# Optimization experiments

Hardware: AMD Instinct MI355X
Metric: run time of the kernel (lower is better)

## Reference

```python
import jax, jax.numpy as jnp
import numpy as np

TAU = 0.7
# Dellar moment flip under x<->y swap: (rho, jy, jx, Pyy, Pxy, Pxx, N, Jy, Jx)
FLIP = np.array([0, 2, 1, 5, 4, 3, 6, 8, 7])


def _dellar_matrices():
    # D2Q9 velocities in lettuce stencil order
    e = np.array([[0, 0], [1, 0], [0, 1], [-1, 0], [0, -1],
                  [1, 1], [-1, 1], [-1, -1], [1, -1]], dtype=np.float64)
    ex, ey = e[:, 0], e[:, 1]
    g = np.array([1, -2, -2, -2, -2, 4, 4, 4, 4], dtype=np.float64)  # Dellar ghost mode
    third = 1.0 / 3.0
    M = np.stack([
        np.ones(9),            # rho
        ex,                    # jx
        ey,                    # jy
        ex * ex - third,       # Pxx - cs^2 rho
        ex * ey,               # Pxy
        ey * ey - third,       # Pyy - cs^2 rho
        g,                     # N (ghost)
        g * ex,                # Jx (ghost)
        g * ey,                # Jy (ghost)
    ])
    return M, np.linalg.inv(M)


def _mlp(x, w1, b1, w2, b2):
    # x: (nx, ny, 9) -> (nx, ny, 1); Linear(9,24) + ReLU + Linear(24,1)
    h = jax.nn.relu(jnp.einsum('xyi,oi->xyo', x, w1) + b1)
    return jnp.einsum('xyo,po->xyp', h, w2) + b2


def setup_inputs() -> dict:
    key = jax.random.key(0)
    ks = jax.random.split(key, 9)
    nx = ny = 2048
    f = jax.random.uniform(ks[0], (9, nx, ny), dtype=jnp.float32)

    def lin_w(k, o, i):
        return jax.random.uniform(k, (o, i), dtype=jnp.float32,
                                  minval=-1.0, maxval=1.0) / np.sqrt(i)

    def lin_b(k, o, i):
        return jax.random.uniform(k, (o,), dtype=jnp.float32,
                                  minval=-1.0, maxval=1.0) / np.sqrt(i)

    M, Minv = _dellar_matrices()
    return {
        'f': f,
        'j_w1': lin_w(ks[1], 24, 9), 'j_b1': lin_b(ks[2], 24, 9),
        'j_w2': lin_w(ks[3], 1, 24), 'j_b2': lin_b(ks[4], 1, 24),
        'n_w1': lin_w(ks[5], 24, 9), 'n_b1': lin_b(ks[6], 24, 9),
        'n_w2': lin_w(ks[7], 1, 24), 'n_b2': lin_b(ks[8], 1, 24),
        'M': jnp.asarray(M, jnp.float32),
        'Minv': jnp.asarray(Minv, jnp.float32),
    }


def reference(f, j_w1, j_b1, j_w2, j_b2, n_w1, n_b1, n_w2, n_b2, M, Minv):
    # moment transform: m_i = M_ij f_j, shape (9, nx, ny)
    m = jnp.einsum('ij,jxy->ixy', M, f)
    mt = jnp.transpose(m, (1, 2, 0))        # (nx, ny, 9)
    mtf = mt[..., FLIP]                     # x<->y flipped moments

    gt_half = lambda a: 0.5 + jnp.exp(a)
    tau_jx = gt_half(_mlp(mt, j_w1, j_b1, j_w2, j_b2))[..., 0]
    tau_jy = gt_half(_mlp(mtf, j_w1, j_b1, j_w2, j_b2))[..., 0]
    tau_n = gt_half(_mlp(mt, n_w1, n_b1, n_w2, n_b2)
                    + _mlp(mtf, n_w1, n_b1, n_w2, n_b2))[..., 0]

    taus = jnp.full_like(m, TAU)
    taus = taus.at[6].set(tau_n).at[7].set(tau_jx).at[8].set(tau_jy)

    rho, jx, jy = m[0], m[1], m[2]
    zero = jnp.zeros_like(rho)
    meq = jnp.stack([rho, jx, jy,
                     jx * jx / rho, jx * jy / rho, jy * jy / rho,
                     zero, zero, zero])

    m_post = m - (m - meq) / taus
    return jnp.einsum('ij,jxy->ixy', Minv, m_post)
```

## Files before the change

### kernel.cpp

```cpp
#include <hip/hip_runtime.h>

typedef float f32x2 __attribute__((ext_vector_type(2)));

__device__ __forceinline__ f32x2 splat2(float s) { f32x2 v; v.x = s; v.y = s; return v; }
__device__ __forceinline__ f32x2 pfma(f32x2 a, f32x2 b, f32x2 c) { return __builtin_elementwise_fma(a, b, c); }
__device__ __forceinline__ f32x2 pfmas(float a, f32x2 b, f32x2 c) { return __builtin_elementwise_fma(splat2(a), b, c); }
__device__ __forceinline__ f32x2 prelu(f32x2 a) { return __builtin_elementwise_max(a, splat2(0.0f)); }

#define NP 2

__global__ __launch_bounds__(256) void mrt_kernel(
    const float* __restrict__ f,
    const float* __restrict__ j_w1, const float* __restrict__ j_b1,
    const float* __restrict__ j_w2, const float* __restrict__ j_b2,
    const float* __restrict__ n_w1, const float* __restrict__ n_b1,
    const float* __restrict__ n_w2, const float* __restrict__ n_b2,
    const float* __restrict__ Mg, const float* __restrict__ Minvg,
    float* __restrict__ out, int n2)
{
    __shared__ __align__(16) float sW[24][20];
    __shared__ float sW2[24][2];
    __shared__ float sMt[9][9];
    __shared__ float sMv[9][9];
    __shared__ float sb2[2];

    const int tid = threadIdx.x;

    if (tid < 48) {
        const int o = tid >> 1;
        const int which = tid & 1;
        const float* w1 = which ? n_w1 : j_w1;
        const float* b1 = which ? n_b1 : j_b1;
        float w[9];
        #pragma unroll
        for (int i = 0; i < 9; ++i) w[i] = w1[o * 9 + i];
        float* dst = &sW[o][which * 10];
        dst[0] = w[0]; dst[1] = w[4]; dst[2] = w[6];
        dst[3] = 0.5f * (w[1] + w[2]); dst[4] = 0.5f * (w[3] + w[5]); dst[5] = 0.5f * (w[7] + w[8]);
        dst[6] = 0.5f * (w[1] - w[2]); dst[7] = 0.5f * (w[3] - w[5]); dst[8] = 0.5f * (w[7] - w[8]);
        dst[9] = b1[o];
        if (which == 0) { sW2[o][0] = j_w2[o]; sW2[o][1] = n_w2[o]; }
    }
    for (int t = tid; t < 81; t += 256) {
        sMt[t % 9][t / 9] = Mg[t];
        sMv[t / 9][t % 9] = Minvg[t];
    }
    if (tid == 0) { sb2[0] = j_b2[0]; sb2[1] = n_b2[0]; }
    __syncthreads();

    const long base = ((long)blockIdx.x * blockDim.x + tid) * (2 * NP);
    if (base >= n2) return;

    f32x2 m[NP][9];
    #pragma unroll
    for (int p = 0; p < NP; ++p)
        #pragma unroll
        for (int r = 0; r < 9; ++r) m[p][r] = splat2(0.0f);

    #pragma unroll
    for (int i = 0; i < 9; ++i) {
        const float4 v = *reinterpret_cast<const float4*>(f + (size_t)i * n2 + base);
        f32x2 v0; v0.x = v.x; v0.y = v.y;
        f32x2 v1; v1.x = v.z; v1.y = v.w;
        #pragma unroll
        for (int r = 0; r < 9; ++r) {
            const float w = sMt[i][r];
            m[0][r] = pfmas(w, v0, m[0][r]);
            m[1][r] = pfmas(w, v1, m[1][r]);
        }
    }

    f32x2 tv[NP][9];
    #pragma unroll
    for (int p = 0; p < NP; ++p) {
        tv[p][0] = m[p][0]; tv[p][1] = m[p][4]; tv[p][2] = m[p][6];
        tv[p][3] = m[p][1] + m[p][2]; tv[p][4] = m[p][3] + m[p][5]; tv[p][5] = m[p][7] + m[p][8];
        tv[p][6] = m[p][1] - m[p][2]; tv[p][7] = m[p][3] - m[p][5]; tv[p][8] = m[p][7] - m[p][8];
    }

    f32x2 accj[NP], accjf[NP], accn[NP];
    #pragma unroll
    for (int p = 0; p < NP; ++p) { accj[p] = splat2(0.f); accjf[p] = splat2(0.f); accn[p] = splat2(0.f); }

    #pragma unroll 4
    for (int o = 0; o < 24; ++o) {
        const float4* pw = reinterpret_cast<const float4*>(sW[o]);
        const float4 c0 = pw[0], c1 = pw[1], c2 = pw[2], c3 = pw[3], c4 = pw[4];
        const float w2j = sW2[o][0], w2n = sW2[o][1];
        #pragma unroll
        for (int p = 0; p < NP; ++p) {
            f32x2 s = splat2(c2.y);
            s = pfmas(c0.x, tv[p][0], s);
            s = pfmas(c0.y, tv[p][1], s);
            s = pfmas(c0.z, tv[p][2], s);
            s = pfmas(c0.w, tv[p][3], s);
            s = pfmas(c1.x, tv[p][4], s);
            s = pfmas(c1.y, tv[p][5], s);
            f32x2 a = splat2(c1.z) * tv[p][6];
            a = pfmas(c1.w, tv[p][7], a);
            a = pfmas(c2.x, tv[p][8], a);
            const f32x2 hj  = prelu(s + a);
            const f32x2 hjf = prelu(s - a);

            f32x2 sn = splat2(c4.w);
            sn = pfmas(c2.z, tv[p][0], sn);
            sn = pfmas(c2.w, tv[p][1], sn);
            sn = pfmas(c3.x, tv[p][2], sn);
            sn = pfmas(c3.y, tv[p][3], sn);
            sn = pfmas(c3.z, tv[p][4], sn);
            sn = pfmas(c3.w, tv[p][5], sn);
            f32x2 an_ = splat2(c4.x) * tv[p][6];
            an_ = pfmas(c4.y, tv[p][7], an_);
            an_ = pfmas(c4.z, tv[p][8], an_);
            const f32x2 hn  = prelu(sn + an_);
            const f32x2 hnf = prelu(sn - an_);

            accj[p]  = pfmas(w2j, hj,  accj[p]);
            accjf[p] = pfmas(w2j, hjf, accjf[p]);
            accn[p]  = pfmas(w2n, hn + hnf, accn[p]);
        }
    }

    const float b2j = sb2[0], b2n = sb2[1];
    const f32x2 Cs = splat2(1.0f / 0.7f);
    #pragma unroll
    for (int p = 0; p < NP; ++p) {
        const f32x2 aj  = accj[p]  + splat2(b2j);
        const f32x2 ajf = accjf[p] + splat2(b2j);
        const f32x2 an  = accn[p]  + splat2(2.0f * b2n);
        f32x2 rt7, rt8, rt6, rrho;
        rt7.x = __builtin_amdgcn_rcpf(0.5f + __expf(aj.x));
        rt7.y = __builtin_amdgcn_rcpf(0.5f + __expf(aj.y));
        rt8.x = __builtin_amdgcn_rcpf(0.5f + __expf(ajf.x));
        rt8.y = __builtin_amdgcn_rcpf(0.5f + __expf(ajf.y));
        rt6.x = __builtin_amdgcn_rcpf(0.5f + __expf(an.x));
        rt6.y = __builtin_amdgcn_rcpf(0.5f + __expf(an.y));
        rrho.x = __builtin_amdgcn_rcpf(m[p][0].x);
        rrho.y = __builtin_amdgcn_rcpf(m[p][0].y);
        const f32x2 jx = m[p][1], jy = m[p][2];
        m[p][3] = m[p][3] - (m[p][3] - jx * jx * rrho) * Cs;
        m[p][4] = m[p][4] - (m[p][4] - jx * jy * rrho) * Cs;
        m[p][5] = m[p][5] - (m[p][5] - jy * jy * rrho) * Cs;
        m[p][6] = m[p][6] - m[p][6] * rt6;
        m[p][7] = m[p][7] - m[p][7] * rt7;
        m[p][8] = m[p][8] - m[p][8] * rt8;
    }

    #pragma unroll
    for (int r = 0; r < 9; ++r) {
        f32x2 o0 = splat2(0.f), o1 = splat2(0.f);
        #pragma unroll
        for (int j = 0; j < 9; ++j) {
            const float w = sMv[r][j];
            o0 = pfmas(w, m[0][j], o0);
            o1 = pfmas(w, m[1][j], o1);
        }
        const float4 vv = make_float4(o0.x, o0.y, o1.x, o1.y);
        *reinterpret_cast<float4*>(out + (size_t)r * n2 + base) = vv;
    }
}

extern "C" void kernel_launch(void* const* d_in, const int* in_sizes, int n_in,
                              void* d_out, int out_size, void* d_ws, size_t ws_size,
                              hipStream_t stream) {
    const float* f    = (const float*)d_in[0];
    const float* j_w1 = (const float*)d_in[1];
    const float* j_b1 = (const float*)d_in[2];
    const float* j_w2 = (const float*)d_in[3];
    const float* j_b2 = (const float*)d_in[4];
    const float* n_w1 = (const float*)d_in[5];
    const float* n_b1 = (const float*)d_in[6];
    const float* n_w2 = (const float*)d_in[7];
    const float* n_b2 = (const float*)d_in[8];
    const float* Mg   = (const float*)d_in[9];
    const float* Minv = (const float*)d_in[10];
    float* out = (float*)d_out;

    const int n2 = in_sizes[0] / 9;
    const int pts_per_block = 256 * 2 * NP;
    const int grid = (n2 + pts_per_block - 1) / pts_per_block;

    mrt_kernel<<<grid, 256, 0, stream>>>(f, j_w1, j_b1, j_w2, j_b2,
                                         n_w1, n_b1, n_w2, n_b2,
                                         Mg, Minv, out, n2);
}
```

Before: 300.2 us.

## Precompute folded weights in prep kernel and use residual-form inverse transform

Splits the work into a tiny prep kernel that writes pre-folded MLP weights, a combined M-then-symmetrize matrix, and negated Minv columns into workspace. The main kernel reads these from global memory (uniform scalar loads) instead of staging them in shared memory with a block barrier. The inverse transform is rewritten as f + Minv*(-delta) over only the six relaxed moments, which drops the rho/j terms and cuts FMAs. It adds a second launch, and it relies on the first three moments being conserved (true for this Minv*M identity).

```diff
diff --git a/kernel.cpp b/kernel.cpp
--- a/kernel.cpp
+++ b/kernel.cpp
@@ -3,128 +3,134 @@
 typedef float f32x2 __attribute__((ext_vector_type(2)));
 
 __device__ __forceinline__ f32x2 splat2(float s) { f32x2 v; v.x = s; v.y = s; return v; }
-__device__ __forceinline__ f32x2 pfma(f32x2 a, f32x2 b, f32x2 c) { return __builtin_elementwise_fma(a, b, c); }
 __device__ __forceinline__ f32x2 pfmas(float a, f32x2 b, f32x2 c) { return __builtin_elementwise_fma(splat2(a), b, c); }
 __device__ __forceinline__ f32x2 prelu(f32x2 a) { return __builtin_elementwise_max(a, splat2(0.0f)); }
 
-#define NP 2
-
-__global__ __launch_bounds__(256) void mrt_kernel(
-    const float* __restrict__ f,
+
+__global__ __launch_bounds__(256) void prep_kernel(
     const float* __restrict__ j_w1, const float* __restrict__ j_b1,
     const float* __restrict__ j_w2, const float* __restrict__ j_b2,
     const float* __restrict__ n_w1, const float* __restrict__ n_b1,
     const float* __restrict__ n_w2, const float* __restrict__ n_b2,
     const float* __restrict__ Mg, const float* __restrict__ Minvg,
-    float* __restrict__ out, int n2)
+    float* __restrict__ ws)
 {
-    __shared__ __align__(16) float sW[24][20];
-    __shared__ float sW2[24][2];
-    __shared__ float sMt[9][9];
-    __shared__ float sMv[9][9];
-    __shared__ float sb2[2];
-
-    const int tid = threadIdx.x;
-
-    if (tid < 48) {
-        const int o = tid >> 1;
-        const int which = tid & 1;
+    const int t = threadIdx.x;
+    if (t < 48) {
+        const int o = t >> 1, which = t & 1;
         const float* w1 = which ? n_w1 : j_w1;
         const float* b1 = which ? n_b1 : j_b1;
         float w[9];
         #pragma unroll
         for (int i = 0; i < 9; ++i) w[i] = w1[o * 9 + i];
-        float* dst = &sW[o][which * 10];
+        float* dst = ws + o * 24 + which * 10;
         dst[0] = w[0]; dst[1] = w[4]; dst[2] = w[6];
         dst[3] = 0.5f * (w[1] + w[2]); dst[4] = 0.5f * (w[3] + w[5]); dst[5] = 0.5f * (w[7] + w[8]);
         dst[6] = 0.5f * (w[1] - w[2]); dst[7] = 0.5f * (w[3] - w[5]); dst[8] = 0.5f * (w[7] - w[8]);
         dst[9] = b1[o];
-        if (which == 0) { sW2[o][0] = j_w2[o]; sW2[o][1] = n_w2[o]; }
-    }
-    for (int t = tid; t < 81; t += 256) {
-        sMt[t % 9][t / 9] = Mg[t];
-        sMv[t / 9][t % 9] = Minvg[t];
-    }
-    if (tid == 0) { sb2[0] = j_b2[0]; sb2[1] = n_b2[0]; }
-    __syncthreads();
-
-    const long base = ((long)blockIdx.x * blockDim.x + tid) * (2 * NP);
-    if (base >= n2) return;
-
-    f32x2 m[NP][9];
-    #pragma unroll
-    for (int p = 0; p < NP; ++p)
-        #pragma unroll
-        for (int r = 0; r < 9; ++r) m[p][r] = splat2(0.0f);
-
+        if (!which) {
+            ws[o * 24 + 20] = j_w2[o];
+            ws[o * 24 + 21] = n_w2[o];
+            ws[o * 24 + 22] = 0.0f;
+            ws[o * 24 + 23] = 0.0f;
+        }
+    } else if (t >= 64 && t < 64 + 81) {
+        const int e = t - 64, r = e / 9, i = e % 9;
+        float v;
+        switch (r) {
+            case 0: v = Mg[0 * 9 + i]; break;
+            case 1: v = Mg[4 * 9 + i]; break;
+            case 2: v = Mg[6 * 9 + i]; break;
+            case 3: v = Mg[1 * 9 + i] + Mg[2 * 9 + i]; break;
+            case 4: v = Mg[3 * 9 + i] + Mg[5 * 9 + i]; break;
+            case 5: v = Mg[7 * 9 + i] + Mg[8 * 9 + i]; break;
+            case 6: v = Mg[1 * 9 + i] - Mg[2 * 9 + i]; break;
+            case 7: v = Mg[3 * 9 + i] - Mg[5 * 9 + i]; break;
+            default: v = Mg[7 * 9 + i] - Mg[8 * 9 + i]; break;
+        }
+        ws[576 + r * 9 + i] = v;
+    } else if (t >= 160 && t < 160 + 54) {
+        const int e = t - 160, r = e / 6, c = e % 6;
+        ws[672 + e] = -Minvg[r * 9 + 3 + c];
+    } else if (t == 254) {
+        ws[728] = j_b2[0];
+    } else if (t == 255) {
+        ws[729] = n_b2[0];
+    }
+}
+
+__global__ __launch_bounds__(256) void mrt_main(
+    const float* __restrict__ f, const float* __restrict__ W,
+    float* __restrict__ out, int n2)
+{
+    long base = ((long)blockIdx.x * 256 + threadIdx.x) * 4;
+    if (base + 4 > n2) base = n2 - 4;
+
+    f32x2 fv[2][9];
+    f32x2 tv[2][9];
     #pragma unroll
     for (int i = 0; i < 9; ++i) {
         const float4 v = *reinterpret_cast<const float4*>(f + (size_t)i * n2 + base);
-        f32x2 v0; v0.x = v.x; v0.y = v.y;
-        f32x2 v1; v1.x = v.z; v1.y = v.w;
+        fv[0][i].x = v.x; fv[0][i].y = v.y;
+        fv[1][i].x = v.z; fv[1][i].y = v.w;
+    }
+    #pragma unroll
+    for (int r = 0; r < 9; ++r) { tv[0][r] = splat2(0.f); tv[1][r] = splat2(0.f); }
+    #pragma unroll
+    for (int i = 0; i < 9; ++i) {
         #pragma unroll
         for (int r = 0; r < 9; ++r) {
-            const float w = sMt[i][r];
-            m[0][r] = pfmas(w, v0, m[0][r]);
-            m[1][r] = pfmas(w, v1, m[1][r]);
-        }
-    }
-
-    f32x2 tv[NP][9];
-    #pragma unroll
-    for (int p = 0; p < NP; ++p) {
-        tv[p][0] = m[p][0]; tv[p][1] = m[p][4]; tv[p][2] = m[p][6];
-        tv[p][3] = m[p][1] + m[p][2]; tv[p][4] = m[p][3] + m[p][5]; tv[p][5] = m[p][7] + m[p][8];
-        tv[p][6] = m[p][1] - m[p][2]; tv[p][7] = m[p][3] - m[p][5]; tv[p][8] = m[p][7] - m[p][8];
-    }
-
-    f32x2 accj[NP], accjf[NP], accn[NP];
-    #pragma unroll
-    for (int p = 0; p < NP; ++p) { accj[p] = splat2(0.f); accjf[p] = splat2(0.f); accn[p] = splat2(0.f); }
+            const float w = W[576 + r * 9 + i];
+            tv[0][r] = pfmas(w, fv[0][i], tv[0][r]);
+            tv[1][r] = pfmas(w, fv[1][i], tv[1][r]);
+        }
+    }
+
+    f32x2 accj[2], accjf[2], accn[2];
+    #pragma unroll
+    for (int p = 0; p < 2; ++p) { accj[p] = splat2(0.f); accjf[p] = splat2(0.f); accn[p] = splat2(0.f); }
 
     #pragma unroll 4
     for (int o = 0; o < 24; ++o) {
-        const float4* pw = reinterpret_cast<const float4*>(sW[o]);
-        const float4 c0 = pw[0], c1 = pw[1], c2 = pw[2], c3 = pw[3], c4 = pw[4];
-        const float w2j = sW2[o][0], w2n = sW2[o][1];
-        #pragma unroll
-        for (int p = 0; p < NP; ++p) {
-            f32x2 s = splat2(c2.y);
-            s = pfmas(c0.x, tv[p][0], s);
-            s = pfmas(c0.y, tv[p][1], s);
-            s = pfmas(c0.z, tv[p][2], s);
-            s = pfmas(c0.w, tv[p][3], s);
-            s = pfmas(c1.x, tv[p][4], s);
-            s = pfmas(c1.y, tv[p][5], s);
-            f32x2 a = splat2(c1.z) * tv[p][6];
-            a = pfmas(c1.w, tv[p][7], a);
-            a = pfmas(c2.x, tv[p][8], a);
-            const f32x2 hj  = prelu(s + a);
-            const f32x2 hjf = prelu(s - a);
-
-            f32x2 sn = splat2(c4.w);
-            sn = pfmas(c2.z, tv[p][0], sn);
-            sn = pfmas(c2.w, tv[p][1], sn);
-            sn = pfmas(c3.x, tv[p][2], sn);
-            sn = pfmas(c3.y, tv[p][3], sn);
-            sn = pfmas(c3.z, tv[p][4], sn);
-            sn = pfmas(c3.w, tv[p][5], sn);
-            f32x2 an_ = splat2(c4.x) * tv[p][6];
-            an_ = pfmas(c4.y, tv[p][7], an_);
-            an_ = pfmas(c4.z, tv[p][8], an_);
-            const f32x2 hn  = prelu(sn + an_);
-            const f32x2 hnf = prelu(sn - an_);
-
-            accj[p]  = pfmas(w2j, hj,  accj[p]);
-            accjf[p] = pfmas(w2j, hjf, accjf[p]);
-            accn[p]  = pfmas(w2n, hn + hnf, accn[p]);
-        }
-    }
-
-    const float b2j = sb2[0], b2n = sb2[1];
-    const f32x2 Cs = splat2(1.0f / 0.7f);
-    #pragma unroll
-    for (int p = 0; p < NP; ++p) {
+        const float* wo = W + o * 24;
+        const float w0 = wo[0], w1 = wo[1], w2 = wo[2], w3 = wo[3], w4 = wo[4], w5 = wo[5];
+        const float a0 = wo[6], a1 = wo[7], a2 = wo[8], b1j = wo[9];
+        const float u0 = wo[10], u1 = wo[11], u2 = wo[12], u3 = wo[13], u4 = wo[14], u5 = wo[15];
+        const float v0 = wo[16], v1 = wo[17], v2 = wo[18], b1n = wo[19];
+        const float w2j = wo[20], w2n = wo[21];
+        #pragma unroll
+        for (int p = 0; p < 2; ++p) {
+            f32x2 s = splat2(b1j);
+            s = pfmas(w0, tv[p][0], s);
+            s = pfmas(w1, tv[p][1], s);
+            s = pfmas(w2, tv[p][2], s);
+            s = pfmas(w3, tv[p][3], s);
+            s = pfmas(w4, tv[p][4], s);
+            s = pfmas(w5, tv[p][5], s);
+            f32x2 a = splat2(a0) * tv[p][6];
+            a = pfmas(a1, tv[p][7], a);
+            a = pfmas(a2, tv[p][8], a);
+            accj[p]  = pfmas(w2j, prelu(s + a), accj[p]);
+            accjf[p] = pfmas(w2j, prelu(s - a), accjf[p]);
+
+            f32x2 sn = splat2(b1n);
+            sn = pfmas(u0, tv[p][0], sn);
+            sn = pfmas(u1, tv[p][1], sn);
+            sn = pfmas(u2, tv[p][2], sn);
+            sn = pfmas(u3, tv[p][3], sn);
+            sn = pfmas(u4, tv[p][4], sn);
+            sn = pfmas(u5, tv[p][5], sn);
+            f32x2 an = splat2(v0) * tv[p][6];
+            an = pfmas(v1, tv[p][7], an);
+            an = pfmas(v2, tv[p][8], an);
+            accn[p] = pfmas(w2n, prelu(sn + an) + prelu(sn - an), accn[p]);
+        }
+    }
+
+    const float b2j = W[728], b2n = W[729];
+    f32x2 d[2][6];
+    #pragma unroll
+    for (int p = 0; p < 2; ++p) {
         const f32x2 aj  = accj[p]  + splat2(b2j);
         const f32x2 ajf = accjf[p] + splat2(b2j);
         const f32x2 an  = accn[p]  + splat2(2.0f * b2n);
@@ -135,25 +141,34 @@
         rt8.y = __builtin_amdgcn_rcpf(0.5f + __expf(ajf.y));
         rt6.x = __builtin_amdgcn_rcpf(0.5f + __expf(an.x));
         rt6.y = __builtin_amdgcn_rcpf(0.5f + __expf(an.y));
-        rrho.x = __builtin_amdgcn_rcpf(m[p][0].x);
-        rrho.y = __builtin_amdgcn_rcpf(m[p][0].y);
-        const f32x2 jx = m[p][1], jy = m[p][2];
-        m[p][3] = m[p][3] - (m[p][3] - jx * jx * rrho) * Cs;
-        m[p][4] = m[p][4] - (m[p][4] - jx * jy * rrho) * Cs;
-        m[p][5] = m[p][5] - (m[p][5] - jy * jy * rrho) * Cs;
-        m[p][6] = m[p][6] - m[p][6] * rt6;
-        m[p][7] = m[p][7] - m[p][7] * rt7;
-        m[p][8] = m[p][8] - m[p][8] * rt8;
+        rrho.x = __builtin_amdgcn_rcpf(tv[p][0].x);
+        rrho.y = __builtin_amdgcn_rcpf(tv[p][0].y);
+
+        const f32x2 jx = splat2(0.5f) * (tv[p][3] + tv[p][6]);
+        const f32x2 jy = splat2(0.5f) * (tv[p][3] - tv[p][6]);
+        const f32x2 m3 = splat2(0.5f) * (tv[p][4] + tv[p][7]);
+        const f32x2 m5 = splat2(0.5f) * (tv[p][4] - tv[p][7]);
+        const f32x2 m7 = splat2(0.5f) * (tv[p][5] + tv[p][8]);
+        const f32x2 m8 = splat2(0.5f) * (tv[p][5] - tv[p][8]);
+        const f32x2 m4 = tv[p][1], m6 = tv[p][2];
+
+        const f32x2 Cs = splat2(1.0f / 0.7f);
+        d[p][0] = (m3 - jx * jx * rrho) * Cs;
+        d[p][1] = (m4 - jx * jy * rrho) * Cs;
+        d[p][2] = (m5 - jy * jy * rrho) * Cs;
+        d[p][3] = m6 * rt6;
+        d[p][4] = m7 * rt7;
+        d[p][5] = m8 * rt8;
     }
 
     #pragma unroll
     for (int r = 0; r < 9; ++r) {
-        f32x2 o0 = splat2(0.f), o1 = splat2(0.f);
-        #pragma unroll
-        for (int j = 0; j < 9; ++j) {
-            const float w = sMv[r][j];
-            o0 = pfmas(w, m[0][j], o0);
-            o1 = pfmas(w, m[1][j], o1);
+        f32x2 o0 = fv[0][r], o1 = fv[1][r];
+        #pragma unroll
+        for (int c = 0; c < 6; ++c) {
+            const float w = W[672 + r * 6 + c];
+            o0 = pfmas(w, d[0][c], o0);
+            o1 = pfmas(w, d[1][c], o1);
         }
         const float4 vv = make_float4(o0.x, o0.y, o1.x, o1.y);
         *reinterpret_cast<float4*>(out + (size_t)r * n2 + base) = vv;
@@ -175,12 +190,13 @@
     const float* Mg   = (const float*)d_in[9];
     const float* Minv = (const float*)d_in[10];
     float* out = (float*)d_out;
+    float* ws  = (float*)d_ws;
 
     const int n2 = in_sizes[0] / 9;
-    const int pts_per_block = 256 * 2 * NP;
+    const int pts_per_block = 256 * 4;
     const int grid = (n2 + pts_per_block - 1) / pts_per_block;
 
-    mrt_kernel<<<grid, 256, 0, stream>>>(f, j_w1, j_b1, j_w2, j_b2,
-                                         n_w1, n_b1, n_w2, n_b2,
-                                         Mg, Minv, out, n2);
+    prep_kernel<<<1, 256, 0, stream>>>(j_w1, j_b1, j_w2, j_b2,
+                                       n_w1, n_b1, n_w2, n_b2, Mg, Minv, ws);
+    mrt_main<<<grid, 256, 0, stream>>>(f, ws, out, n2);
 }
```

Result: no change. 303.9 us (+1.2%).
